# Optimization experiments

Hardware: AMD Instinct MI355X
Metric: run time of the kernel (lower is better)

Reference implementation:

```python
import jax, jax.numpy as jnp
import numpy as np

B, N, F_DIM, E, C = 8, 16384, 64, 262144, 10
BN_EPS = 1e-5


def setup_inputs() -> dict:
    key = jax.random.key(0)
    ks = jax.random.split(key, 10)
    s = 1.0 / np.sqrt(F_DIM)
    return {
        "x": jax.random.normal(ks[0], (B, N, F_DIM), jnp.float32),
        "edge_src": jax.random.randint(ks[1], (B, E), 0, N, jnp.int32),
        "edge_dst": jax.random.randint(ks[2], (B, E), 0, N, jnp.int32),
        "W1": jax.random.normal(ks[3], (F_DIM, F_DIM), jnp.float32) * s,
        "b1": jax.random.normal(ks[4], (F_DIM,), jnp.float32) * 0.01,
        "W2": jax.random.normal(ks[5], (F_DIM, F_DIM), jnp.float32) * s,
        "b2": jax.random.normal(ks[6], (F_DIM,), jnp.float32) * 0.01,
        "bn_gamma": jnp.ones((F_DIM,), jnp.float32),
        "bn_beta": jnp.zeros((F_DIM,), jnp.float32),
        "lin_W": jax.random.normal(ks[7], (C, N * F_DIM), jnp.float32) * (1.0 / np.sqrt(N * F_DIM)),
        "lin_b": jax.random.normal(ks[8], (C,), jnp.float32) * 0.01,
    }


def _graph_conv(x, src, dst, W, b):
    # DGL GraphConv, norm='both', in_feats == out_feats (aggregate-first path):
    # h = D_in^{-1/2} * A * (D_out^{-1/2} * x) @ W + b, degrees clamped to >= 1.
    ones = jnp.ones((src.shape[0],), x.dtype)
    deg_out = jnp.maximum(jax.ops.segment_sum(ones, src, num_segments=N), 1.0)
    deg_in = jnp.maximum(jax.ops.segment_sum(ones, dst, num_segments=N), 1.0)
    xs = x * jax.lax.rsqrt(deg_out)[:, None]          # [N, F]
    agg = jax.ops.segment_sum(xs[src], dst, num_segments=N)  # gather + scatter-add
    rst = agg * jax.lax.rsqrt(deg_in)[:, None]
    return rst @ W + b


def reference(x, edge_src, edge_dst, W1, b1, W2, b2, bn_gamma, bn_beta, lin_W, lin_b):
    conv = jax.vmap(_graph_conv, in_axes=(0, 0, 0, None, None))
    h = jax.nn.relu(conv(x, edge_src, edge_dst, W1, b1))  # conv1 + relu
    # dropout p=0.0 (eval): identity
    h = conv(h, edge_src, edge_dst, W2, b2)               # conv2 -> [B, N, F]
    # BatchNorm1d over channel F (torch normalizes over B and N in training mode)
    mean = jnp.mean(h, axis=(0, 1))
    var = jnp.var(h, axis=(0, 1))
    h = bn_gamma * (h - mean) * jax.lax.rsqrt(var + BN_EPS) + bn_beta
    flat = h.reshape(B, N * F_DIM)
    return flat @ lin_W.T + lin_b                         # [B, C]
```

## Files before the change

kernel.cpp:

```cpp
#include <hip/hip_runtime.h>

#define B_     8
#define N_     16384
#define F_     64
#define E_     262144
#define C_     10
#define NF_    (N_ * F_)
#define BN_    (B_ * N_)
#define BNF_   (B_ * N_ * F_)
#define BE_    (B_ * E_)
#define CAP_   48
#define CHUNK_ 4096
#define NCH_   (E_ / CHUNK_)
#define NW_    (N_ / 4)
#define NSB_   4096
#define NFB_   1024
#define EPS_   1e-5f

typedef _Float16 h8 __attribute__((ext_vector_type(8)));
typedef _Float16 h4 __attribute__((ext_vector_type(4)));
typedef float f32x4 __attribute__((ext_vector_type(4)));

#define SWZ(r, o) ((((r) * 64 + (o))) ^ (((r) & 7) << 3))

__global__ __launch_bounds__(256) void k_count(const int* __restrict__ src,
                                               const int* __restrict__ dst,
                                               unsigned int* __restrict__ partO,
                                               unsigned int* __restrict__ partI,
                                               const float* __restrict__ W1,
                                               const float* __restrict__ W2,
                                               _Float16* __restrict__ Wt1,
                                               _Float16* __restrict__ Wt2) {
    __shared__ unsigned int pO[NW_];
    __shared__ unsigned int pI[NW_];
    int t = threadIdx.x;
    if (blockIdx.x >= B_ * NCH_) {
        int g = blockIdx.x - B_ * NCH_;
        const float* Ws = (g & 8) ? W2 : W1;
        _Float16* Wd = (g & 8) ? Wt2 : Wt1;
        int c0 = (g & 7) * 512;
        for (int j = t; j < 512; j += 256) {
            int o = c0 + j;
            Wd[o] = (_Float16)Ws[(o & 63) * 64 + (o >> 6)];
        }
        return;
    }
    int b = blockIdx.x & 7, c = blockIdx.x >> 3;
    for (int i = t; i < NW_; i += 256) { pO[i] = 0; pI[i] = 0; }
    __syncthreads();
    const int* sb = src + (size_t)b * E_ + (size_t)c * CHUNK_;
    const int* db = dst + (size_t)b * E_ + (size_t)c * CHUNK_;
    for (int i = t; i < CHUNK_; i += 256) {
        int s = sb[i], d = db[i];
        atomicAdd(&pO[s >> 2], 1u << ((s & 3) * 8));
        atomicAdd(&pI[d >> 2], 1u << ((d & 3) * 8));
    }
    __syncthreads();
    size_t base = (size_t)(b * NCH_ + c) * NW_;
    for (int i = t; i < NW_; i += 256) {
        partO[base + i] = pO[i];
        partI[base + i] = pI[i];
    }
}

__global__ __launch_bounds__(256) void k_offsets(const unsigned int* __restrict__ partO,
                                                 const unsigned int* __restrict__ partI,
                                                 unsigned int* __restrict__ baseArr,
                                                 float* __restrict__ degOr,
                                                 float* __restrict__ degIr,
                                                 int* __restrict__ cntI_g) {
    int gw = blockIdx.x * 256 + threadIdx.x;
    int b = gw >> 12;
    int rw = gw & 4095;
    unsigned int sumI = 0, sumO = 0;
    for (int c = 0; c < NCH_; ++c) {
        size_t idx = (size_t)(b * NCH_ + c) * NW_ + rw;
        unsigned int wI = partI[idx];
        baseArr[idx] = sumI;
        sumI += wI;
        sumO += partO[idx];
    }
    int row0 = gw * 4;
#pragma unroll
    for (int r = 0; r < 4; ++r) {
        unsigned int ci = (sumI >> (r * 8)) & 0xFFu;
        unsigned int co = (sumO >> (r * 8)) & 0xFFu;
        degIr[row0 + r] = rsqrtf(fmaxf((float)ci, 1.0f));
        degOr[row0 + r] = rsqrtf(fmaxf((float)co, 1.0f));
        cntI_g[row0 + r] = (int)ci;
    }
}

__global__ __launch_bounds__(256) void k_fill(const int* __restrict__ src,
                                              const int* __restrict__ dst,
                                              const unsigned int* __restrict__ baseArr,
                                              unsigned short* __restrict__ csr) {
    __shared__ unsigned int cur[NW_];
    __shared__ unsigned int bw[NW_];
    int t = threadIdx.x;
    int b = blockIdx.x & 7, c = blockIdx.x >> 3;
    size_t pbase = (size_t)(b * NCH_ + c) * NW_;
    for (int i = t; i < NW_; i += 256) { cur[i] = 0; bw[i] = baseArr[pbase + i]; }
    __syncthreads();
    const int* sb = src + (size_t)b * E_ + (size_t)c * CHUNK_;
    const int* db = dst + (size_t)b * E_ + (size_t)c * CHUNK_;
    unsigned short* cb = csr + (size_t)b * N_ * CAP_;
    for (int i = t; i < CHUNK_; i += 256) {
        int s = sb[i], d = db[i];
        unsigned int sh = (d & 3) * 8;
        unsigned int old = atomicAdd(&cur[d >> 2], 1u << sh);
        unsigned int pos = ((old >> sh) & 0xFFu) + ((bw[d >> 2] >> sh) & 0xFFu);
        if (pos < CAP_) cb[d * CAP_ + pos] = (unsigned short)s;
    }
}

template <bool IN16, bool SCALE>
__global__ __launch_bounds__(256) void k_mmf(const float* __restrict__ in32,
                                             const _Float16* __restrict__ in16,
                                             const _Float16* __restrict__ Wt,
                                             const float* __restrict__ rs,
                                             _Float16* __restrict__ out) {
    __shared__ _Float16 Al[4096];
    __shared__ _Float16 Bl[4096];
    int t = threadIdx.x;
    int bat = blockIdx.x & 7;
    int rowg = bat * N_ + (blockIdx.x >> 3) * 64;

#pragma unroll
    for (int j = 0; j < 2; ++j) {
        int c = t + j * 256;
        int r = c >> 3, o = (c & 7) * 8;
        *(h8*)&Al[SWZ(r, o)] = *(const h8*)(Wt + c * 8);
    }
#pragma unroll
    for (int j = 0; j < 2; ++j) {
        int c = t + j * 256;
        int r = c >> 3, o = (c & 7) * 8;
        h8 v;
        if constexpr (IN16) {
            v = *(const h8*)(in16 + (size_t)(rowg + r) * 64 + o);
        } else {
            const float4* p = (const float4*)(in32 + (size_t)(rowg + r) * 64 + o);
            float4 x0 = p[0], x1 = p[1];
            v[0] = (_Float16)x0.x; v[1] = (_Float16)x0.y;
            v[2] = (_Float16)x0.z; v[3] = (_Float16)x0.w;
            v[4] = (_Float16)x1.x; v[5] = (_Float16)x1.y;
            v[6] = (_Float16)x1.z; v[7] = (_Float16)x1.w;
        }
        *(h8*)&Bl[SWZ(r, o)] = v;
    }
    __syncthreads();

    int lane = t & 63;
    int w = t >> 6;
    int lm = lane & 15;
    int lk = (lane >> 4) * 8;
    f32x4 acc0 = {0.f, 0.f, 0.f, 0.f}, acc1 = {0.f, 0.f, 0.f, 0.f};
    f32x4 acc2 = {0.f, 0.f, 0.f, 0.f}, acc3 = {0.f, 0.f, 0.f, 0.f};
#pragma unroll
    for (int ks = 0; ks < 2; ++ks) {
        h8 a = *(const h8*)&Al[SWZ(w * 16 + lm, lk + ks * 32)];
        h8 vb0 = *(const h8*)&Bl[SWZ(0 + lm, lk + ks * 32)];
        h8 vb1 = *(const h8*)&Bl[SWZ(16 + lm, lk + ks * 32)];
        h8 vb2 = *(const h8*)&Bl[SWZ(32 + lm, lk + ks * 32)];
        h8 vb3 = *(const h8*)&Bl[SWZ(48 + lm, lk + ks * 32)];
        acc0 = __builtin_amdgcn_mfma_f32_16x16x32_f16(a, vb0, acc0, 0, 0, 0);
        acc1 = __builtin_amdgcn_mfma_f32_16x16x32_f16(a, vb1, acc1, 0, 0, 0);
        acc2 = __builtin_amdgcn_mfma_f32_16x16x32_f16(a, vb2, acc2, 0, 0, 0);
        acc3 = __builtin_amdgcn_mfma_f32_16x16x32_f16(a, vb3, acc3, 0, 0, 0);
    }
    int fo = w * 16 + (lane >> 4) * 4;
#define STORE_TILE(ACC, RT)                                                    \
    {                                                                          \
        int row = rowg + (RT) * 16 + lm;                                       \
        float scv = SCALE ? rs[row] : 1.0f;                                    \
        h4 ov;                                                                 \
        ov[0] = (_Float16)(ACC[0] * scv); ov[1] = (_Float16)(ACC[1] * scv);    \
        ov[2] = (_Float16)(ACC[2] * scv); ov[3] = (_Float16)(ACC[3] * scv);    \
        *(h4*)(out + (size_t)row * 64 + fo) = ov;                              \
    }
    STORE_TILE(acc0, 0)
    STORE_TILE(acc1, 1)
    STORE_TILE(acc2, 2)
    STORE_TILE(acc3, 3)
#undef STORE_TILE
}

template <bool CONV1>
__global__ __launch_bounds__(256, 6) void k_gat(
        const int* __restrict__ cnt, const unsigned short* __restrict__ csr,
        const _Float16* __restrict__ z, const float* __restrict__ degIr,
        const float* __restrict__ degOr, const float* __restrict__ bias,
        _Float16* __restrict__ out16, float* __restrict__ pstat) {
    __shared__ float sS[4][64];
    __shared__ float sQ[4][64];
    int t = threadIdx.x;
    int lane = t & 63;
    int wave = t >> 6;
    int c8 = lane & 7;
    int b = blockIdx.x & 7;
    int row = (blockIdx.x >> 3) * 32 + wave * 8 + (lane >> 3);
    int wid = b * N_ + row;
    const _Float16* zb = z + (size_t)b * NF_;
    int lb = lane & 56;
    int ho = c8 * 8;

    int n = cnt[wid];
    if (n > CAP_) n = CAP_;
    size_t cb = (size_t)wid * CAP_;
    int e0 = csr[cb + c8] & 0x3FFF;
    int e1 = csr[cb + 8 + c8] & 0x3FFF;
    int e2 = csr[cb + 16 + c8] & 0x3FFF;
    int e3 = csr[cb + 24 + c8] & 0x3FFF;
    int e4 = csr[cb + 32 + c8] & 0x3FFF;
    int e5 = csr[cb + 40 + c8] & 0x3FFF;
    float dIr = degIr[wid];
    float4 bv0 = *(const float4*)(bias + ho);
    float4 bv1 = *(const float4*)(bias + ho + 4);
    int m = n;
    m = max(m, __shfl_xor(m, 8));
    m = max(m, __shfl_xor(m, 16));
    m = max(m, __shfl_xor(m, 32));

    float af[8];
#pragma unroll
    for (int i = 0; i < 8; ++i) af[i] = 0.0f;

#define SEG(EREG, KOFF)                                                        \
    {                                                                          \
        int rem = n - (KOFF);                                                  \
        h8 v[8];                                                               \
        _Pragma("unroll")                                                      \
        for (int jj = 0; jj < 8; ++jj) {                                       \
            int s = __shfl(EREG, lb + jj);                                     \
            h8 vv = {};                                                        \
            if (jj < rem) vv = *(const h8*)(zb + s * 64 + ho);                 \
            v[jj] = vv;                                                        \
        }                                                                      \
        h8 s0 = v[0] + v[1], s1 = v[2] + v[3];                                 \
        h8 s2 = v[4] + v[5], s3 = v[6] + v[7];                                 \
        h8 s4 = s0 + s1, s5 = s2 + s3;                                         \
        h8 s6 = s4 + s5;                                                       \
        _Pragma("unroll")                                                      \
        for (int i = 0; i < 8; ++i) af[i] += (float)s6[i];                     \
    }

    SEG(e0, 0)
    if (m > 8)  SEG(e1, 8)
    if (m > 16) SEG(e2, 16)
    if (m > 24) SEG(e3, 24)
    if (m > 32) SEG(e4, 32)
    if (m > 40) SEG(e5, 40)
#undef SEG

    float bb[8] = {bv0.x, bv0.y, bv0.z, bv0.w, bv1.x, bv1.y, bv1.z, bv1.w};
    if constexpr (CONV1) {
        float po = degOr[wid];
        h8 ov;
#pragma unroll
        for (int i = 0; i < 8; ++i) {
            ov[i] = (_Float16)(fmaxf(fmaf(af[i], dIr, bb[i]), 0.0f) * po);
        }
        *(h8*)(out16 + (size_t)wid * 64 + ho) = ov;
    } else {
        float vv[8];
        h8 ov;
#pragma unroll
        for (int i = 0; i < 8; ++i) {
            vv[i] = fmaf(af[i], dIr, bb[i]);
            ov[i] = (_Float16)vv[i];
        }
        *(h8*)(out16 + (size_t)wid * 64 + ho) = ov;
        float ssv[8], qqv[8];
#pragma unroll
        for (int i = 0; i < 8; ++i) { ssv[i] = vv[i]; qqv[i] = vv[i] * vv[i]; }
#pragma unroll
        for (int i = 0; i < 8; ++i) {
            ssv[i] += __shfl_xor(ssv[i], 8);  qqv[i] += __shfl_xor(qqv[i], 8);
            ssv[i] += __shfl_xor(ssv[i], 16); qqv[i] += __shfl_xor(qqv[i], 16);
            ssv[i] += __shfl_xor(ssv[i], 32); qqv[i] += __shfl_xor(qqv[i], 32);
        }
        if (lane < 8) {
#pragma unroll
            for (int i = 0; i < 8; ++i) {
                sS[wave][lane * 8 + i] = ssv[i];
                sQ[wave][lane * 8 + i] = qqv[i];
            }
        }
        __syncthreads();
        if (t < 64) {
            float s_ = sS[0][t] + sS[1][t] + sS[2][t] + sS[3][t];
            float q_ = sQ[0][t] + sQ[1][t] + sQ[2][t] + sQ[3][t];
            pstat[(size_t)blockIdx.x * 128 + t] = s_;
            pstat[(size_t)blockIdx.x * 128 + 64 + t] = q_;
        }
    }
}

__global__ __launch_bounds__(256) void k_red(const float* __restrict__ part,
                                             float* __restrict__ stats2) {
    __shared__ float sred[256];
    int t = threadIdx.x;
    int half = t >> 7;
    int s = t & 127;
    int r0 = blockIdx.x * (NSB_ / 32);
    float acc = 0.0f;
    for (int k = 0; k < NSB_ / 32 / 2; ++k) {
        acc += part[(size_t)(r0 + k * 2 + half) * 128 + s];
    }
    sred[t] = acc;
    __syncthreads();
    if (t < 128) stats2[blockIdx.x * 128 + t] = sred[t] + sred[t + 128];
}

__global__ __launch_bounds__(256) void k_final(
        const _Float16* __restrict__ h, const float* __restrict__ linW,
        const float* __restrict__ stats2, const float* __restrict__ gamma,
        const float* __restrict__ beta, float* __restrict__ pf) {
    __shared__ float scs[64], shs[64];
    int t = threadIdx.x;
    if (t < 64) {
        float sum = 0.0f, sq = 0.0f;
#pragma unroll
        for (int j = 0; j < 32; ++j) {
            sum += stats2[j * 128 + t];
            sq  += stats2[j * 128 + 64 + t];
        }
        float inv = 1.0f / (float)BN_;
        float mean = sum * inv;
        float var  = sq * inv - mean * mean;
        float s = gamma[t] * rsqrtf(var + EPS_);
        scs[t] = s;
        shs[t] = beta[t] - mean * s;
    }
    __syncthreads();

    int lane = t & 63;
    int wv = t >> 6;
    int b0 = wv * 2, b1 = wv * 2 + 1;
    int base = blockIdx.x * (NF_ / NFB_);
    float4 s4  = *(const float4*)&scs[(lane & 15) * 4];
    float4 sh4 = *(const float4*)&shs[(lane & 15) * 4];
    float acc[C_][2];
#pragma unroll
    for (int c = 0; c < C_; ++c) { acc[c][0] = 0.0f; acc[c][1] = 0.0f; }

#pragma unroll
    for (int k = 0; k < 4; ++k) {
        int i = base + k * 256 + lane * 4;
        h4 ha = *(const h4*)(h + (size_t)b0 * NF_ + i);
        h4 hb = *(const h4*)(h + (size_t)b1 * NF_ + i);
        float h0[4], h1[4];
        h0[0] = fmaf((float)ha[0], s4.x, sh4.x);
        h0[1] = fmaf((float)ha[1], s4.y, sh4.y);
        h0[2] = fmaf((float)ha[2], s4.z, sh4.z);
        h0[3] = fmaf((float)ha[3], s4.w, sh4.w);
        h1[0] = fmaf((float)hb[0], s4.x, sh4.x);
        h1[1] = fmaf((float)hb[1], s4.y, sh4.y);
        h1[2] = fmaf((float)hb[2], s4.z, sh4.z);
        h1[3] = fmaf((float)hb[3], s4.w, sh4.w);
#pragma unroll
        for (int c = 0; c < C_; ++c) {
            float4 w4 = *(const float4*)(linW + (size_t)c * NF_ + i);
            float a0 = acc[c][0], a1 = acc[c][1];
            a0 = fmaf(h0[0], w4.x, a0); a0 = fmaf(h0[1], w4.y, a0);
            a0 = fmaf(h0[2], w4.z, a0); a0 = fmaf(h0[3], w4.w, a0);
            a1 = fmaf(h1[0], w4.x, a1); a1 = fmaf(h1[1], w4.y, a1);
            a1 = fmaf(h1[2], w4.z, a1); a1 = fmaf(h1[3], w4.w, a1);
            acc[c][0] = a0; acc[c][1] = a1;
        }
    }

#pragma unroll
    for (int c = 0; c < C_; ++c) {
#pragma unroll
        for (int j = 0; j < 2; ++j) {
            float v = acc[c][j];
            v += __shfl_down(v, 32);
            v += __shfl_down(v, 16);
            v += __shfl_down(v, 8);
            v += __shfl_down(v, 4);
            v += __shfl_down(v, 2);
            v += __shfl_down(v, 1);
            acc[c][j] = v;
        }
    }
    if (lane == 0) {
        float* p = pf + (size_t)blockIdx.x * 80;
#pragma unroll
        for (int c = 0; c < C_; ++c) {
            p[b0 * C_ + c] = acc[c][0];
            p[b1 * C_ + c] = acc[c][1];
        }
    }
}

__global__ __launch_bounds__(64) void k_fsum(const float* __restrict__ pf,
                                             const float* __restrict__ linb,
                                             float* __restrict__ out) {
    int o = blockIdx.x;
    int lane = threadIdx.x;
    float acc = 0.0f;
#pragma unroll
    for (int k = 0; k < 16; ++k) {
        acc += pf[(size_t)(k * 64 + lane) * 80 + o];
    }
    acc += __shfl_down(acc, 32);
    acc += __shfl_down(acc, 16);
    acc += __shfl_down(acc, 8);
    acc += __shfl_down(acc, 4);
    acc += __shfl_down(acc, 2);
    acc += __shfl_down(acc, 1);
    if (lane == 0) out[o] = acc + linb[o % C_];
}

extern "C" void kernel_launch(void* const* d_in, const int* in_sizes, int n_in,
                              void* d_out, int out_size, void* d_ws, size_t ws_size,
                              hipStream_t stream) {
    const float* x        = (const float*)d_in[0];
    const int*   edge_src = (const int*)d_in[1];
    const int*   edge_dst = (const int*)d_in[2];
    const float* W1       = (const float*)d_in[3];
    const float* b1       = (const float*)d_in[4];
    const float* W2       = (const float*)d_in[5];
    const float* b2       = (const float*)d_in[6];
    const float* gamma    = (const float*)d_in[7];
    const float* beta     = (const float*)d_in[8];
    const float* linW     = (const float*)d_in[9];
    const float* linb     = (const float*)d_in[10];
    float* out = (float*)d_out;

    char* w = (char*)d_ws;
    float* degOr = (float*)w;           w += BN_ * 4;
    float* degIr = (float*)w;           w += BN_ * 4;
    int*   cntI  = (int*)w;             w += BN_ * 4;
    unsigned short* csr = (unsigned short*)w; w += (size_t)BN_ * CAP_ * 2;
    _Float16* z    = (_Float16*)w;      w += (size_t)BNF_ * 2;
    _Float16* h1z  = (_Float16*)w;      w += (size_t)BNF_ * 2;
    _Float16* h2h  = (_Float16*)w;      w += (size_t)BNF_ * 2;
    unsigned int* partO   = (unsigned int*)w;  w += (size_t)B_ * NCH_ * NW_ * 4;
    unsigned int* partI   = (unsigned int*)w;  w += (size_t)B_ * NCH_ * NW_ * 4;
    unsigned int* baseArr = (unsigned int*)w;  w += (size_t)B_ * NCH_ * NW_ * 4;
    float* partStats = (float*)w;       w += (size_t)NSB_ * 128 * 4;
    float* stats2 = (float*)w;          w += 32 * 128 * 4;
    float* pf    = (float*)w;           w += (size_t)NFB_ * 80 * 4;
    _Float16* Wt1 = (_Float16*)w;       w += 4096 * 2;
    _Float16* Wt2 = (_Float16*)w;       w += 4096 * 2;

    k_count<<<B_ * NCH_ + 16, 256, 0, stream>>>(edge_src, edge_dst, partO, partI,
                                                W1, W2, Wt1, Wt2);
    k_offsets<<<BN_ / 4 / 256, 256, 0, stream>>>(partO, partI, baseArr, degOr, degIr, cntI);
    k_fill<<<B_ * NCH_, 256, 0, stream>>>(edge_src, edge_dst, baseArr, csr);

    k_mmf<false, true><<<BN_ / 64, 256, 0, stream>>>(x, nullptr, Wt1, degOr, z);
    k_gat<true><<<BN_ / 32, 256, 0, stream>>>(cntI, csr, z, degIr, degOr, b1, h1z, nullptr);

    k_mmf<true, false><<<BN_ / 64, 256, 0, stream>>>(nullptr, h1z, Wt2, nullptr, z);
    k_gat<false><<<BN_ / 32, 256, 0, stream>>>(cntI, csr, z, degIr, nullptr, b2, h2h, partStats);

    k_red<<<32, 256, 0, stream>>>(partStats, stats2);
    k_final<<<NFB_, 256, 0, stream>>>(h2h, linW, stats2, gamma, beta, pf);
    k_fsum<<<80, 64, 0, stream>>>(pf, linb, out);
}
```

Measured before the change: 240.0 us.

## Vectorize edge loads, pack CSR index loads, fuse final sum via ticket

Doubles the edge chunk size and reads src/dst as int4 in the count and fill kernels. The gather kernel now loads CSR neighbour indices as one uint4 per lane and unpacks them from shuffles, and it defers the bias and degree loads until after aggregation. The separate final-sum kernel is removed: the last block of k_final, picked by an atomic ticket, reduces the partials, which drops one launch and adds a memset. The larger chunk halves block count in count/fill but doubles each block's work. The int4 cast assumes the edge arrays are 16-byte aligned.

```diff
diff --git a/kernel.cpp b/kernel.cpp
--- a/kernel.cpp
+++ b/kernel.cpp
@@ -10,7 +10,7 @@
 #define BNF_   (B_ * N_ * F_)
 #define BE_    (B_ * E_)
 #define CAP_   48
-#define CHUNK_ 4096
+#define CHUNK_ 8192
 #define NCH_   (E_ / CHUNK_)
 #define NW_    (N_ / 4)
 #define NSB_   4096
@@ -48,12 +48,19 @@
     int b = blockIdx.x & 7, c = blockIdx.x >> 3;
     for (int i = t; i < NW_; i += 256) { pO[i] = 0; pI[i] = 0; }
     __syncthreads();
-    const int* sb = src + (size_t)b * E_ + (size_t)c * CHUNK_;
-    const int* db = dst + (size_t)b * E_ + (size_t)c * CHUNK_;
-    for (int i = t; i < CHUNK_; i += 256) {
-        int s = sb[i], d = db[i];
-        atomicAdd(&pO[s >> 2], 1u << ((s & 3) * 8));
-        atomicAdd(&pI[d >> 2], 1u << ((d & 3) * 8));
+    const int4* sb = (const int4*)(src + (size_t)b * E_ + (size_t)c * CHUNK_);
+    const int4* db = (const int4*)(dst + (size_t)b * E_ + (size_t)c * CHUNK_);
+#pragma unroll
+    for (int j = 0; j < CHUNK_ / 1024; ++j) {
+        int4 s4 = sb[t + j * 256];
+        int4 d4 = db[t + j * 256];
+#pragma unroll
+        for (int k = 0; k < 4; ++k) {
+            int s = ((const int*)&s4)[k];
+            int d = ((const int*)&d4)[k];
+            atomicAdd(&pO[s >> 2], 1u << ((s & 3) * 8));
+            atomicAdd(&pI[d >> 2], 1u << ((d & 3) * 8));
+        }
     }
     __syncthreads();
     size_t base = (size_t)(b * NCH_ + c) * NW_;
@@ -102,15 +109,22 @@
     size_t pbase = (size_t)(b * NCH_ + c) * NW_;
     for (int i = t; i < NW_; i += 256) { cur[i] = 0; bw[i] = baseArr[pbase + i]; }
     __syncthreads();
-    const int* sb = src + (size_t)b * E_ + (size_t)c * CHUNK_;
-    const int* db = dst + (size_t)b * E_ + (size_t)c * CHUNK_;
+    const int4* sb = (const int4*)(src + (size_t)b * E_ + (size_t)c * CHUNK_);
+    const int4* db = (const int4*)(dst + (size_t)b * E_ + (size_t)c * CHUNK_);
     unsigned short* cb = csr + (size_t)b * N_ * CAP_;
-    for (int i = t; i < CHUNK_; i += 256) {
-        int s = sb[i], d = db[i];
-        unsigned int sh = (d & 3) * 8;
-        unsigned int old = atomicAdd(&cur[d >> 2], 1u << sh);
-        unsigned int pos = ((old >> sh) & 0xFFu) + ((bw[d >> 2] >> sh) & 0xFFu);
-        if (pos < CAP_) cb[d * CAP_ + pos] = (unsigned short)s;
+#pragma unroll
+    for (int j = 0; j < CHUNK_ / 1024; ++j) {
+        int4 s4 = sb[t + j * 256];
+        int4 d4 = db[t + j * 256];
+#pragma unroll
+        for (int k = 0; k < 4; ++k) {
+            int s = ((const int*)&s4)[k];
+            int d = ((const int*)&d4)[k];
+            unsigned int sh = (d & 3) * 8;
+            unsigned int old = atomicAdd(&cur[d >> 2], 1u << sh);
+            unsigned int pos = ((old >> sh) & 0xFFu) + ((bw[d >> 2] >> sh) & 0xFFu);
+            if (pos < CAP_) cb[(size_t)d * CAP_ + pos] = (unsigned short)s;
+        }
     }
 }
 
@@ -208,15 +222,8 @@
     int n = cnt[wid];
     if (n > CAP_) n = CAP_;
     size_t cb = (size_t)wid * CAP_;
-    int e0 = csr[cb + c8] & 0x3FFF;
-    int e1 = csr[cb + 8 + c8] & 0x3FFF;
-    int e2 = csr[cb + 16 + c8] & 0x3FFF;
-    int e3 = csr[cb + 24 + c8] & 0x3FFF;
-    int e4 = csr[cb + 32 + c8] & 0x3FFF;
-    int e5 = csr[cb + 40 + c8] & 0x3FFF;
-    float dIr = degIr[wid];
-    float4 bv0 = *(const float4*)(bias + ho);
-    float4 bv1 = *(const float4*)(bias + ho + 4);
+    uint4 ev = {0u, 0u, 0u, 0u};
+    if (c8 < 6) ev = *(const uint4*)(csr + cb + c8 * 8);
     int m = n;
     m = max(m, __shfl_xor(m, 8));
     m = max(m, __shfl_xor(m, 16));
@@ -226,13 +233,17 @@
 #pragma unroll
     for (int i = 0; i < 8; ++i) af[i] = 0.0f;
 
-#define SEG(EREG, KOFF)                                                        \
+#define SEG(KOFF)                                                              \
     {                                                                          \
         int rem = n - (KOFF);                                                  \
+        int srcl = lb + ((KOFF) >> 3);                                         \
+        unsigned dd0 = __shfl(ev.x, srcl), dd1 = __shfl(ev.y, srcl);           \
+        unsigned dd2 = __shfl(ev.z, srcl), dd3 = __shfl(ev.w, srcl);           \
+        unsigned dd[4] = {dd0, dd1, dd2, dd3};                                 \
         h8 v[8];                                                               \
         _Pragma("unroll")                                                      \
         for (int jj = 0; jj < 8; ++jj) {                                       \
-            int s = __shfl(EREG, lb + jj);                                     \
+            int s = (int)((dd[jj >> 1] >> ((jj & 1) * 16)) & 0x3FFFu);         \
             h8 vv = {};                                                        \
             if (jj < rem) vv = *(const h8*)(zb + s * 64 + ho);                 \
             v[jj] = vv;                                                        \
@@ -245,14 +256,17 @@
         for (int i = 0; i < 8; ++i) af[i] += (float)s6[i];                     \
     }
 
-    SEG(e0, 0)
-    if (m > 8)  SEG(e1, 8)
-    if (m > 16) SEG(e2, 16)
-    if (m > 24) SEG(e3, 24)
-    if (m > 32) SEG(e4, 32)
-    if (m > 40) SEG(e5, 40)
+    SEG(0)
+    if (m > 8)  SEG(8)
+    if (m > 16) SEG(16)
+    if (m > 24) SEG(24)
+    if (m > 32) SEG(32)
+    if (m > 40) SEG(40)
 #undef SEG
 
+    float dIr = degIr[wid];
+    float4 bv0 = *(const float4*)(bias + ho);
+    float4 bv1 = *(const float4*)(bias + ho + 4);
     float bb[8] = {bv0.x, bv0.y, bv0.z, bv0.w, bv1.x, bv1.y, bv1.z, bv1.w};
     if constexpr (CONV1) {
         float po = degOr[wid];
@@ -316,8 +330,12 @@
 __global__ __launch_bounds__(256) void k_final(
         const _Float16* __restrict__ h, const float* __restrict__ linW,
         const float* __restrict__ stats2, const float* __restrict__ gamma,
-        const float* __restrict__ beta, float* __restrict__ pf) {
+        const float* __restrict__ beta, float* __restrict__ pf,
+        const float* __restrict__ linb, float* __restrict__ out,
+        unsigned int* __restrict__ ticket) {
     __shared__ float scs[64], shs[64];
+    __shared__ float fs[160];
+    __shared__ int amLast;
     int t = threadIdx.x;
     if (t < 64) {
         float sum = 0.0f, sq = 0.0f;
@@ -393,25 +411,24 @@
             p[b1 * C_ + c] = acc[c][1];
         }
     }
-}
-
-__global__ __launch_bounds__(64) void k_fsum(const float* __restrict__ pf,
-                                             const float* __restrict__ linb,
-                                             float* __restrict__ out) {
-    int o = blockIdx.x;
-    int lane = threadIdx.x;
-    float acc = 0.0f;
-#pragma unroll
-    for (int k = 0; k < 16; ++k) {
-        acc += pf[(size_t)(k * 64 + lane) * 80 + o];
-    }
-    acc += __shfl_down(acc, 32);
-    acc += __shfl_down(acc, 16);
-    acc += __shfl_down(acc, 8);
-    acc += __shfl_down(acc, 4);
-    acc += __shfl_down(acc, 2);
-    acc += __shfl_down(acc, 1);
-    if (lane == 0) out[o] = acc + linb[o % C_];
+
+    __threadfence();
+    __syncthreads();
+    if (t == 0) amLast = (atomicAdd(ticket, 1u) == NFB_ - 1);
+    __syncthreads();
+    if (amLast) {
+        __threadfence();
+        if (t < 160) {
+            int o = t % 80, half = t / 80;
+            const float* pp = pf + (size_t)half * (NFB_ / 2) * 80 + o;
+            float a = 0.0f;
+#pragma unroll 8
+            for (int k = 0; k < NFB_ / 2; ++k) a += pp[(size_t)k * 80];
+            fs[t] = a;
+        }
+        __syncthreads();
+        if (t < 80) out[t] = fs[t] + fs[t + 80] + linb[t % C_];
+    }
 }
 
 extern "C" void kernel_launch(void* const* d_in, const int* in_sizes, int n_in,
@@ -446,6 +463,9 @@
     float* pf    = (float*)w;           w += (size_t)NFB_ * 80 * 4;
     _Float16* Wt1 = (_Float16*)w;       w += 4096 * 2;
     _Float16* Wt2 = (_Float16*)w;       w += 4096 * 2;
+    unsigned int* ticket = (unsigned int*)w; w += 64;
+
+    hipMemsetAsync(ticket, 0, 4, stream);
 
     k_count<<<B_ * NCH_ + 16, 256, 0, stream>>>(edge_src, edge_dst, partO, partI,
                                                 W1, W2, Wt1, Wt2);
@@ -459,6 +479,6 @@
     k_gat<false><<<BN_ / 32, 256, 0, stream>>>(cntI, csr, z, degIr, nullptr, b2, h2h, partStats);
 
     k_red<<<32, 256, 0, stream>>>(partStats, stats2);
-    k_final<<<NFB_, 256, 0, stream>>>(h2h, linW, stats2, gamma, beta, pf);
-    k_fsum<<<80, 64, 0, stream>>>(pf, linb, out);
-}
+    k_final<<<NFB_, 256, 0, stream>>>(h2h, linW, stats2, gamma, beta, pf,
+                                      linb, out, ticket);
+}
```

Result: slower. 343.4 us (+43.0%).
